# Kernel tuning notes

Hardware: AMD Instinct MI355X
Metric: run time of the kernel (lower is better)

The kernel has to match this reference:

```python
import jax, jax.numpy as jnp
import numpy as np

HIDDEN = 768
HEADS = 12
HEAD_DIM = HIDDEN // HEADS
SCALE = HEAD_DIM ** -0.5
B, S = 8, 1024


def _qkv(x, Wqkv):
    # x: [b, s, H] -> q, k, v each [b, heads, s, d]
    h = jnp.einsum('bsh,hk->bsk', x, Wqkv)          # [b, s, 3*H]
    h = h.reshape(x.shape[0], x.shape[1], 3, HEADS, HEAD_DIM)
    h = jnp.transpose(h, (2, 0, 3, 1, 4))           # [3, b, heads, s, d]
    return h[0], h[1], h[2]


def _attn(q, k, v):
    # q,k,v: [b, heads, s, d]
    att = jax.nn.softmax(jnp.einsum('bhxd,bhyd->bhxy', q, k) * SCALE, axis=-1)
    return jnp.einsum('bhxy,bhyd->bhxd', att, v)


def _out(o, Wout, bout):
    # o: [b, heads, s, d] -> [b, s, H]
    b, h, s, d = o.shape
    o = jnp.transpose(o, (0, 2, 1, 3)).reshape(b, s, h * d)
    return jnp.einsum('bsh,hk->bsk', o, Wout) + bout


def setup_inputs() -> dict:
    key = jax.random.key(0)
    k1, k2, k3, k4, k5 = jax.random.split(key, 5)
    x = jax.random.normal(k1, (B, S, HIDDEN), dtype=jnp.float32)
    x2 = jax.random.normal(k2, (B, S, HIDDEN), dtype=jnp.float32)
    Wqkv = jax.random.normal(k3, (HIDDEN, 3 * HIDDEN), dtype=jnp.float32) * (HIDDEN ** -0.5)
    Wout = jax.random.normal(k4, (HIDDEN, HIDDEN), dtype=jnp.float32) * (HIDDEN ** -0.5)
    bout = jax.random.normal(k5, (HIDDEN,), dtype=jnp.float32) * 0.01
    return {'x': x, 'x2': x2, 'Wqkv': Wqkv, 'Wout': Wout, 'bout': bout}


def reference(x, x2, Wqkv, Wout, bout):
    q, k, v = _qkv(x, Wqkv)
    q2, k2, v2 = _qkv(x2, Wqkv)
    o1 = _attn(q, k, v)      # self-attention on x
    o2 = _attn(q2, k2, v2)   # self-attention on x2
    o3 = _attn(q, k2, v2)    # cross-attention: queries from x, keys/values from x2
    y1 = _out(o1, Wout, bout)
    y2 = _out(o2, Wout, bout)
    y3 = _out(o3, Wout, bout)
    return (y1, y2, y3)
```

## Files before the change

### kernel.cpp

```cpp
#include <hip/hip_runtime.h>
#include <math.h>


#define HIDDEN 768
#define NH 12
#define HD 64
#define BB 8
#define SS 1024
#define ATT_SCALE 0.125f

typedef unsigned short u16;
typedef unsigned int u32;
typedef __attribute__((ext_vector_type(8))) short short8;
typedef __attribute__((ext_vector_type(4))) float f32x4;

constexpr int MROWS = BB * SS;
constexpr int M_QKV = 2 * MROWS;
constexpr int N_QKV = 3 * HIDDEN;
constexpr long QKV_ELEMS = (long)BB * NH * SS * HD;
constexpr long AX_ELEMS  = (long)M_QKV * HIDDEN;
constexpr long O_ELEMS   = (long)3 * MROWS * HIDDEN;
constexpr long WQT_ELEMS = (long)N_QKV * HIDDEN;
constexpr size_t OFF2 = (size_t)12 * QKV_ELEMS * 2;

__device__ inline u16 f2bf(float x) {
    u32 u = __float_as_uint(x);
    return (u16)((u + 0x7FFFu + ((u >> 16) & 1u)) >> 16);
}
__device__ inline float bf2f(u16 h) { return __uint_as_float(((u32)h) << 16); }
__device__ inline int swz(int row, int bcol) {
    return ((row << 7) + bcol) ^ ((row & 7) << 4);
}
__device__ inline int swzV(int row, int bcol) {
    return ((row << 7) + bcol) ^ ((((row >> 3) ^ row) & 7) << 4);
}
#define MFMA16(a, b, c) __builtin_amdgcn_mfma_f32_16x16x32_bf16(a, b, c, 0, 0, 0)

__device__ inline void gload16(const u16* g, u16* l) {
    __builtin_amdgcn_global_load_lds(
        (const __attribute__((address_space(1))) u32*)g,
        (__attribute__((address_space(3))) u32*)l, 16, 0, 0);
}

__global__ __launch_bounds__(256) void conv_x_kernel(
    const float* __restrict__ x, const float* __restrict__ x2,
    u16* __restrict__ axh, u16* __restrict__ axl)
{
    const size_t HALF = (size_t)MROWS * HIDDEN;
    const size_t NTOT = (size_t)AX_ELEMS;
    const size_t step = (size_t)gridDim.x * 256 * 4;
    for (size_t e = ((size_t)blockIdx.x * 256 + threadIdx.x) * 4; e < NTOT; e += step) {
        const float4 v = (e < HALF) ? *(const float4*)&x[e]
                                    : *(const float4*)&x2[e - HALF];
        ushort4 h, l;
        h.x = f2bf(v.x); l.x = f2bf(v.x - bf2f(h.x));
        h.y = f2bf(v.y); l.y = f2bf(v.y - bf2f(h.y));
        h.z = f2bf(v.z); l.z = f2bf(v.z - bf2f(h.z));
        h.w = f2bf(v.w); l.w = f2bf(v.w - bf2f(h.w));
        *(ushort4*)&axh[e] = h;
        *(ushort4*)&axl[e] = l;
    }
}

__global__ __launch_bounds__(256) void conv_wt_kernel(
    const float* __restrict__ Wqkv, const float* __restrict__ Wout,
    u16* __restrict__ wqt_h, u16* __restrict__ wqt_l,
    u16* __restrict__ wot_h, u16* __restrict__ wot_l)
{
    __shared__ float T[64][65];
    const int bk = blockIdx.x;
    int bn = blockIdx.y;
    const float* W; int ncols; u16 *oh, *ol;
    if (bn < 36) { W = Wqkv; ncols = N_QKV; oh = wqt_h; ol = wqt_l; }
    else         { W = Wout; ncols = HIDDEN; oh = wot_h; ol = wot_l; bn -= 36; }
    const int k0 = bk * 64, n0 = bn * 64;
    const int t = threadIdx.x;
    {
        const int r = t >> 2, c0 = (t & 3) * 16;
        #pragma unroll
        for (int q = 0; q < 4; ++q) {
            const float4 v = *(const float4*)&W[(size_t)(k0 + r) * ncols + n0 + c0 + q * 4];
            T[r][c0 + q * 4 + 0] = v.x;
            T[r][c0 + q * 4 + 1] = v.y;
            T[r][c0 + q * 4 + 2] = v.z;
            T[r][c0 + q * 4 + 3] = v.w;
        }
    }
    __syncthreads();
    {
        const int n = t >> 2, kk0 = (t & 3) * 16;
        const size_t ob = (size_t)(n0 + n) * HIDDEN + k0 + kk0;
        #pragma unroll
        for (int q = 0; q < 4; ++q) {
            ushort4 h, l;
            float v0 = T[kk0 + q * 4 + 0][n];
            float v1 = T[kk0 + q * 4 + 1][n];
            float v2 = T[kk0 + q * 4 + 2][n];
            float v3 = T[kk0 + q * 4 + 3][n];
            h.x = f2bf(v0); l.x = f2bf(v0 - bf2f(h.x));
            h.y = f2bf(v1); l.y = f2bf(v1 - bf2f(h.y));
            h.z = f2bf(v2); l.z = f2bf(v2 - bf2f(h.z));
            h.w = f2bf(v3); l.w = f2bf(v3 - bf2f(h.w));
            *(ushort4*)&oh[ob + q * 4] = h;
            *(ushort4*)&ol[ob + q * 4] = l;
        }
    }
}

__global__ __launch_bounds__(256)
__attribute__((amdgpu_waves_per_eu(2, 2)))
void gemm_qkv_mfma(const u16* __restrict__ Agh, const u16* __restrict__ Agl,
                   const u16* __restrict__ Bgh, const u16* __restrict__ Bgl,
                   u16* __restrict__ planes)
{
    __shared__ u16 LAh[4096], LAl[4096], LBh[4096], LBl[4096];

    const int tid = threadIdx.x, lane = tid & 63, wid = tid >> 6;
    const int l15 = lane & 15, lg = lane >> 4;
    const int wr = wid >> 1, wc = wid & 1;
    const int m0 = blockIdx.x * 128, n0 = blockIdx.y * 128;

    const f32x4 fz = {0.f, 0.f, 0.f, 0.f};
    f32x4 acc[4][4] = {{fz,fz,fz,fz},{fz,fz,fz,fz},{fz,fz,fz,fz},{fz,fz,fz,fz}};

    for (int kt = 0; kt < HIDDEN / 32; ++kt) {
        const int k0 = kt * 32;
        __syncthreads();
        #pragma unroll
        for (int u = 0; u < 2; ++u) {
            const int s   = (wid * 2 + u) * 64 + lane;
            const int row = s >> 2;
            const int kc  = (s & 3) * 8;
            const int lo  = (wid * 2 + u) * 512;
            const size_t ga = (size_t)(m0 + row) * HIDDEN + k0 + kc;
            const size_t gb = (size_t)(n0 + row) * HIDDEN + k0 + kc;
            gload16(Agh + ga, &LAh[lo]);
            gload16(Agl + ga, &LAl[lo]);
            gload16(Bgh + gb, &LBh[lo]);
            gload16(Bgl + gb, &LBl[lo]);
        }
        __syncthreads();

        short8 ah[4], al[4], bh[4], bl[4];
        #pragma unroll
        for (int i = 0; i < 4; ++i) {
            const int ro = (wr * 64 + i * 16 + l15) * 32 + lg * 8;
            ah[i] = *(const short8*)&LAh[ro];
            al[i] = *(const short8*)&LAl[ro];
        }
        #pragma unroll
        for (int j = 0; j < 4; ++j) {
            const int ro = (wc * 64 + j * 16 + l15) * 32 + lg * 8;
            bh[j] = *(const short8*)&LBh[ro];
            bl[j] = *(const short8*)&LBl[ro];
        }
        #pragma unroll
        for (int i = 0; i < 4; ++i)
            #pragma unroll
            for (int j = 0; j < 4; ++j) {
                acc[i][j] = MFMA16(ah[i], bh[j], acc[i][j]);
                acc[i][j] = MFMA16(ah[i], bl[j], acc[i][j]);
                acc[i][j] = MFMA16(al[i], bh[j], acc[i][j]);
            }
    }

    #pragma unroll
    for (int i = 0; i < 4; ++i) {
        #pragma unroll
        for (int r = 0; r < 4; ++r) {
            const int mr  = m0 + wr * 64 + i * 16 + lg * 4 + r;
            const int inp = (mr >= MROWS) ? 1 : 0;
            const int mm  = mr & (MROWS - 1);
            const int bb  = mm >> 10, ssr = mm & (SS - 1);
            #pragma unroll
            for (int j = 0; j < 4; ++j) {
                const int n   = n0 + wc * 64 + j * 16 + l15;
                const int sel = n / HIDDEN;
                const int hh  = (n % HIDDEN) >> 6;
                const int dd  = n & 63;
                const float v = acc[i][j][r];
                const u16 vh = f2bf(v);
                const u16 vl = f2bf(v - bf2f(vh));
                u16* ph = planes + (size_t)(inp * 6 + sel * 2) * QKV_ELEMS;
                const size_t idx = (((size_t)bb * NH + hh) * SS + ssr) * HD + dd;
                ph[idx] = vh;
                ph[QKV_ELEMS + idx] = vl;
            }
        }
    }
}

__global__ __launch_bounds__(256)
__attribute__((amdgpu_waves_per_eu(2, 2)))
void attn_mfma_kernel(const u16* __restrict__ planes,
                      u16* __restrict__ o_h, u16* __restrict__ o_l)
{
    __shared__ u16 Khi[64 * 64], Klo[64 * 64];
    __shared__ u16 Vthi[64 * 64], Vtlo[64 * 64];
    __shared__ u16 Pbuf[4][2][2][16 * 64];

    const int tid  = threadIdx.x;
    const int lane = tid & 63, wid = tid >> 6;
    const int l15  = lane & 15, lg = lane >> 4;

    const int work = (blockIdx.x & 7) * 288 + (blockIdx.x >> 3);
    const int qt   = work & 7;
    const int bh   = (work >> 3) % 96;
    const int aid  = (work >> 3) / 96;

    const int qinp  = (aid == 1) ? 1 : 0;
    const int kvinp = (aid == 0) ? 0 : 1;
    const size_t base = (size_t)bh * SS * HD;

    const u16* __restrict__ qhi = planes + (size_t)(qinp * 6 + 0) * QKV_ELEMS;
    const u16* __restrict__ qlo = qhi + QKV_ELEMS;
    const u16* __restrict__ khi = planes + (size_t)(kvinp * 6 + 2) * QKV_ELEMS;
    const u16* __restrict__ klo = khi + QKV_ELEMS;
    const u16* __restrict__ vhi = planes + (size_t)(kvinp * 6 + 4) * QKV_ELEMS;
    const u16* __restrict__ vlo = vhi + QKV_ELEMS;

    const int qb = qt * 128 + wid * 32;
    short8 qfh[2][2], qfl[2][2];
    #pragma unroll
    for (int g = 0; g < 2; ++g)
        #pragma unroll
        for (int dk = 0; dk < 2; ++dk) {
            const size_t off = base + (size_t)(qb + g * 16 + l15) * HD + dk * 32 + lg * 8;
            qfh[g][dk] = *(const short8*)&qhi[off];
            qfl[g][dk] = *(const short8*)&qlo[off];
        }

    const f32x4 fz = {0.f, 0.f, 0.f, 0.f};
    f32x4 O[2][4] = {{fz, fz, fz, fz}, {fz, fz, fz, fz}};
    float mrun[2] = {-INFINITY, -INFINITY};
    float lrun[2] = {0.f, 0.f};

    for (int kt0 = 0; kt0 < SS; kt0 += 64) {
        __syncthreads();
        {
            #pragma unroll
            for (int i = 0; i < 2; ++i) {
                const int c  = tid + 256 * i;
                const int ky = c >> 3, dg = (c & 7) * 8;
                const size_t g = base + (size_t)(kt0 + ky) * HD + dg;
                const int b = swz(ky, dg * 2);
                *(short8*)((char*)Khi + b) = *(const short8*)&khi[g];
                *(short8*)((char*)Klo + b) = *(const short8*)&klo[g];
            }
            const int kp = tid >> 3;
            const int d0 = (tid & 7) * 8;
            const size_t g0 = base + (size_t)(kt0 + 2 * kp) * HD + d0;
            short8 vah = *(const short8*)&vhi[g0];
            short8 vbh = *(const short8*)&vhi[g0 + HD];
            short8 val = *(const short8*)&vlo[g0];
            short8 vbl = *(const short8*)&vlo[g0 + HD];
            #pragma unroll
            for (int i = 0; i < 8; ++i) {
                const int d = d0 + i;
                const int b = swzV(d, kp * 4);
                *(u32*)((char*)Vthi + b) = (u32)(u16)vah[i] | ((u32)(u16)vbh[i] << 16);
                *(u32*)((char*)Vtlo + b) = (u32)(u16)val[i] | ((u32)(u16)vbl[i] << 16);
            }
        }
        __syncthreads();

        f32x4 S[2][4] = {{fz, fz, fz, fz}, {fz, fz, fz, fz}};
        #pragma unroll
        for (int dk = 0; dk < 2; ++dk) {
            #pragma unroll
            for (int kt = 0; kt < 4; ++kt) {
                const int b = swz(kt * 16 + l15, dk * 64 + lg * 16);
                short8 kfh = *(const short8*)((char*)Khi + b);
                short8 kfl = *(const short8*)((char*)Klo + b);
                #pragma unroll
                for (int g = 0; g < 2; ++g) {
                    S[g][kt] = MFMA16(kfh, qfh[g][dk], S[g][kt]);
                    S[g][kt] = MFMA16(kfl, qfh[g][dk], S[g][kt]);
                    S[g][kt] = MFMA16(kfh, qfl[g][dk], S[g][kt]);
                }
            }
        }

        #pragma unroll
        for (int g = 0; g < 2; ++g) {
            float pm = -INFINITY;
            #pragma unroll
            for (int kt = 0; kt < 4; ++kt)
                #pragma unroll
                for (int r = 0; r < 4; ++r) {
                    S[g][kt][r] *= ATT_SCALE;
                    pm = fmaxf(pm, S[g][kt][r]);
                }
            pm = fmaxf(pm, __shfl_xor(pm, 16, 64));
            pm = fmaxf(pm, __shfl_xor(pm, 32, 64));
            const float mnew = fmaxf(mrun[g], pm);
            const float corr = __expf(mrun[g] - mnew);
            mrun[g] = mnew;
            lrun[g] *= corr;

            u16* __restrict__ Ph = &Pbuf[wid][g][0][0];
            u16* __restrict__ Pl = &Pbuf[wid][g][1][0];
            float psum = 0.f;
            #pragma unroll
            for (int kt = 0; kt < 4; ++kt) {
                float p0 = __expf(S[g][kt][0] - mnew);
                float p1 = __expf(S[g][kt][1] - mnew);
                float p2 = __expf(S[g][kt][2] - mnew);
                float p3 = __expf(S[g][kt][3] - mnew);
                psum += (p0 + p1) + (p2 + p3);
                const u32 u0 = __float_as_uint(p0), u1 = __float_as_uint(p1);
                const u32 u2 = __float_as_uint(p2), u3 = __float_as_uint(p3);
                const u32 hpk0 = (u0 >> 16) | (u1 & 0xFFFF0000u);
                const u32 hpk1 = (u2 >> 16) | (u3 & 0xFFFF0000u);
                const float l0 = p0 - __uint_as_float(u0 & 0xFFFF0000u);
                const float l1 = p1 - __uint_as_float(u1 & 0xFFFF0000u);
                const float l2 = p2 - __uint_as_float(u2 & 0xFFFF0000u);
                const float l3 = p3 - __uint_as_float(u3 & 0xFFFF0000u);
                const u32 lpk0 = (__float_as_uint(l0) >> 16) | (__float_as_uint(l1) & 0xFFFF0000u);
                const u32 lpk1 = (__float_as_uint(l2) >> 16) | (__float_as_uint(l3) & 0xFFFF0000u);
                const int b0 = swz(l15, kt * 32 + lg * 8);
                *(u32*)((char*)Ph + b0)     = hpk0;
                *(u32*)((char*)Ph + b0 + 4) = hpk1;
                *(u32*)((char*)Pl + b0)     = lpk0;
                *(u32*)((char*)Pl + b0 + 4) = lpk1;
            }
            psum += __shfl_xor(psum, 16, 64);
            psum += __shfl_xor(psum, 32, 64);
            lrun[g] += psum;

            #pragma unroll
            for (int r = 0; r < 4; ++r) {
                const float c = __shfl(corr, lg * 4 + r, 64);
                #pragma unroll
                for (int dn = 0; dn < 4; ++dn) O[g][dn][r] *= c;
            }
        }

        #pragma unroll
        for (int ch = 0; ch < 2; ++ch) {
            short8 vfh[4], vfl[4];
            #pragma unroll
            for (int dn = 0; dn < 4; ++dn) {
                const int vb = swzV(dn * 16 + l15, ch * 64 + lg * 16);
                vfh[dn] = *(const short8*)((char*)Vthi + vb);
                vfl[dn] = *(const short8*)((char*)Vtlo + vb);
            }
            #pragma unroll
            for (int g = 0; g < 2; ++g) {
                const int pb = swz(l15, ch * 64 + lg * 16);
                short8 pah = *(const short8*)((char*)&Pbuf[wid][g][0][0] + pb);
                short8 pal = *(const short8*)((char*)&Pbuf[wid][g][1][0] + pb);
                #pragma unroll
                for (int dn = 0; dn < 4; ++dn) {
                    O[g][dn] = MFMA16(pah, vfh[dn], O[g][dn]);
                    O[g][dn] = MFMA16(pah, vfl[dn], O[g][dn]);
                    O[g][dn] = MFMA16(pal, vfh[dn], O[g][dn]);
                }
            }
        }
    }

    const int b = bh / NH, h = bh % NH;
    #pragma unroll
    for (int g = 0; g < 2; ++g) {
        const float linv = 1.f / lrun[g];
        #pragma unroll
        for (int r = 0; r < 4; ++r) {
            const float inv = __shfl(linv, lg * 4 + r, 64);
            const int grow = aid * MROWS + b * SS + qb + g * 16 + lg * 4 + r;
            const size_t rb = (size_t)grow * HIDDEN + h * HD;
            #pragma unroll
            for (int dn = 0; dn < 4; ++dn) {
                const float v = O[g][dn][r] * inv;
                const u16 vh = f2bf(v);
                o_h[rb + dn * 16 + l15] = vh;
                o_l[rb + dn * 16 + l15] = f2bf(v - bf2f(vh));
            }
        }
    }
}

__global__ __launch_bounds__(256)
__attribute__((amdgpu_waves_per_eu(2, 2)))
void gemm_out_mfma(const u16* __restrict__ Agh, const u16* __restrict__ Agl,
                   const u16* __restrict__ Bgh, const u16* __restrict__ Bgl,
                   const float* __restrict__ bias, float* __restrict__ out)
{
    __shared__ u16 LAh[4096], LAl[4096], LBh[4096], LBl[4096];

    const int tid = threadIdx.x, lane = tid & 63, wid = tid >> 6;
    const int l15 = lane & 15, lg = lane >> 4;
    const int wr = wid >> 1, wc = wid & 1;
    const int m0 = blockIdx.x * 128, n0 = blockIdx.y * 128;

    const f32x4 fz = {0.f, 0.f, 0.f, 0.f};
    f32x4 acc[4][4] = {{fz,fz,fz,fz},{fz,fz,fz,fz},{fz,fz,fz,fz},{fz,fz,fz,fz}};

    for (int kt = 0; kt < HIDDEN / 32; ++kt) {
        const int k0 = kt * 32;
        __syncthreads();
        #pragma unroll
        for (int u = 0; u < 2; ++u) {
            const int s   = (wid * 2 + u) * 64 + lane;
            const int row = s >> 2;
            const int kc  = (s & 3) * 8;
            const int lo  = (wid * 2 + u) * 512;
            const size_t ga = (size_t)(m0 + row) * HIDDEN + k0 + kc;
            const size_t gb = (size_t)(n0 + row) * HIDDEN + k0 + kc;
            gload16(Agh + ga, &LAh[lo]);
            gload16(Agl + ga, &LAl[lo]);
            gload16(Bgh + gb, &LBh[lo]);
            gload16(Bgl + gb, &LBl[lo]);
        }
        __syncthreads();

        short8 ah[4], al[4], bh[4], bl[4];
        #pragma unroll
        for (int i = 0; i < 4; ++i) {
            const int ro = (wr * 64 + i * 16 + l15) * 32 + lg * 8;
            ah[i] = *(const short8*)&LAh[ro];
            al[i] = *(const short8*)&LAl[ro];
        }
        #pragma unroll
        for (int j = 0; j < 4; ++j) {
            const int ro = (wc * 64 + j * 16 + l15) * 32 + lg * 8;
            bh[j] = *(const short8*)&LBh[ro];
            bl[j] = *(const short8*)&LBl[ro];
        }
        #pragma unroll
        for (int i = 0; i < 4; ++i)
            #pragma unroll
            for (int j = 0; j < 4; ++j) {
                acc[i][j] = MFMA16(ah[i], bh[j], acc[i][j]);
                acc[i][j] = MFMA16(ah[i], bl[j], acc[i][j]);
                acc[i][j] = MFMA16(al[i], bh[j], acc[i][j]);
            }
    }

    #pragma unroll
    for (int i = 0; i < 4; ++i) {
        #pragma unroll
        for (int r = 0; r < 4; ++r) {
            const int mr = m0 + wr * 64 + i * 16 + lg * 4 + r;
            #pragma unroll
            for (int j = 0; j < 4; ++j) {
                const int n = n0 + wc * 64 + j * 16 + l15;
                out[(size_t)mr * HIDDEN + n] = acc[i][j][r] + bias[n];
            }
        }
    }
}

extern "C" void kernel_launch(void* const* d_in, const int* in_sizes, int n_in,
                              void* d_out, int out_size, void* d_ws, size_t ws_size,
                              hipStream_t stream)
{
    const float* x    = (const float*)d_in[0];
    const float* x2   = (const float*)d_in[1];
    const float* Wqkv = (const float*)d_in[2];
    const float* Wout = (const float*)d_in[3];
    const float* bout = (const float*)d_in[4];
    float* out = (float*)d_out;

    char* wsb = (char*)d_ws;
    u16* planes = (u16*)wsb;
    u16* ax_h  = (u16*)(wsb + OFF2);
    u16* ax_l  = ax_h + AX_ELEMS;
    u16* wqt_h = ax_l + AX_ELEMS;
    u16* wqt_l = wqt_h + WQT_ELEMS;
    u16* o_h   = (u16*)(wsb + OFF2);
    u16* o_l   = o_h + O_ELEMS;
    u16* wot_h = o_l + O_ELEMS;
    u16* wot_l = wot_h + (long)HIDDEN * HIDDEN;

    conv_x_kernel<<<3072, 256, 0, stream>>>(x, x2, ax_h, ax_l);

    dim3 gw(12, 48);
    conv_wt_kernel<<<gw, 256, 0, stream>>>(Wqkv, Wout, wqt_h, wqt_l, wot_h, wot_l);

    dim3 g1(M_QKV / 128, N_QKV / 128);
    gemm_qkv_mfma<<<g1, 256, 0, stream>>>(ax_h, ax_l, wqt_h, wqt_l, planes);

    attn_mfma_kernel<<<2304, 256, 0, stream>>>(planes, o_h, o_l);

    dim3 g3(3 * MROWS / 128, HIDDEN / 128);
    gemm_out_mfma<<<g3, 256, 0, stream>>>(o_h, o_l, wot_h, wot_l, bout, out);
}
```

Measured before the change: 662.4 us.

## Double-buffer GEMM LDS tiles and add lazy softmax rescaling in attention

Both projection GEMMs now use two LDS buffers, issuing the next K-tile's global-to-LDS loads before the current tile's MFMAs, with one barrier per iteration. The attention kernel now rescales the running max and output accumulator only when some row's new max exceeds the stored one by more than 8, which skips the per-tile exp and shuffle rescale work. P-tile stores are also merged into 64-bit writes. Costs: the GEMM LDS footprint doubles, which may limit occupancy. The lazy rescale lets exponentials reach up to e^8 before renormalising, which shifts the split-bf16 precision of P slightly.

Measured after the change: 702.4 us. 1.06x slower.

```diff
diff --git a/kernel.cpp b/kernel.cpp
--- a/kernel.cpp
+++ b/kernel.cpp
@@ -113,19 +113,15 @@
                    const u16* __restrict__ Bgh, const u16* __restrict__ Bgl,
                    u16* __restrict__ planes)
 {
-    __shared__ u16 LAh[4096], LAl[4096], LBh[4096], LBl[4096];
+    __shared__ u16 LAh[2][4096], LAl[2][4096], LBh[2][4096], LBl[2][4096];
 
     const int tid = threadIdx.x, lane = tid & 63, wid = tid >> 6;
     const int l15 = lane & 15, lg = lane >> 4;
     const int wr = wid >> 1, wc = wid & 1;
     const int m0 = blockIdx.x * 128, n0 = blockIdx.y * 128;
 
-    const f32x4 fz = {0.f, 0.f, 0.f, 0.f};
-    f32x4 acc[4][4] = {{fz,fz,fz,fz},{fz,fz,fz,fz},{fz,fz,fz,fz},{fz,fz,fz,fz}};
-
-    for (int kt = 0; kt < HIDDEN / 32; ++kt) {
+    auto stage = [&](int kt, int bf) {
         const int k0 = kt * 32;
-        __syncthreads();
         #pragma unroll
         for (int u = 0; u < 2; ++u) {
             const int s   = (wid * 2 + u) * 64 + lane;
@@ -134,25 +130,35 @@
             const int lo  = (wid * 2 + u) * 512;
             const size_t ga = (size_t)(m0 + row) * HIDDEN + k0 + kc;
             const size_t gb = (size_t)(n0 + row) * HIDDEN + k0 + kc;
-            gload16(Agh + ga, &LAh[lo]);
-            gload16(Agl + ga, &LAl[lo]);
-            gload16(Bgh + gb, &LBh[lo]);
-            gload16(Bgl + gb, &LBl[lo]);
-        }
-        __syncthreads();
+            gload16(Agh + ga, &LAh[bf][lo]);
+            gload16(Agl + ga, &LAl[bf][lo]);
+            gload16(Bgh + gb, &LBh[bf][lo]);
+            gload16(Bgl + gb, &LBl[bf][lo]);
+        }
+    };
+
+    const f32x4 fz = {0.f, 0.f, 0.f, 0.f};
+    f32x4 acc[4][4] = {{fz,fz,fz,fz},{fz,fz,fz,fz},{fz,fz,fz,fz},{fz,fz,fz,fz}};
+
+    stage(0, 0);
+    __syncthreads();
+
+    int bf = 0;
+    for (int kt = 0; kt < HIDDEN / 32; ++kt) {
+        if (kt + 1 < HIDDEN / 32) stage(kt + 1, bf ^ 1);
 
         short8 ah[4], al[4], bh[4], bl[4];
         #pragma unroll
         for (int i = 0; i < 4; ++i) {
             const int ro = (wr * 64 + i * 16 + l15) * 32 + lg * 8;
-            ah[i] = *(const short8*)&LAh[ro];
-            al[i] = *(const short8*)&LAl[ro];
+            ah[i] = *(const short8*)&LAh[bf][ro];
+            al[i] = *(const short8*)&LAl[bf][ro];
         }
         #pragma unroll
         for (int j = 0; j < 4; ++j) {
             const int ro = (wc * 64 + j * 16 + l15) * 32 + lg * 8;
-            bh[j] = *(const short8*)&LBh[ro];
-            bl[j] = *(const short8*)&LBl[ro];
+            bh[j] = *(const short8*)&LBh[bf][ro];
+            bl[j] = *(const short8*)&LBl[bf][ro];
         }
         #pragma unroll
         for (int i = 0; i < 4; ++i)
@@ -162,6 +168,8 @@
                 acc[i][j] = MFMA16(ah[i], bl[j], acc[i][j]);
                 acc[i][j] = MFMA16(al[i], bh[j], acc[i][j]);
             }
+        __syncthreads();
+        bf ^= 1;
     }
 
     #pragma unroll
@@ -293,20 +301,30 @@
                 }
             pm = fmaxf(pm, __shfl_xor(pm, 16, 64));
             pm = fmaxf(pm, __shfl_xor(pm, 32, 64));
-            const float mnew = fmaxf(mrun[g], pm);
-            const float corr = __expf(mrun[g] - mnew);
-            mrun[g] = mnew;
-            lrun[g] *= corr;
+
+            if (__any(pm - mrun[g] > 8.f)) {
+                const float mnew = fmaxf(mrun[g], pm);
+                const float corr = __expf(mrun[g] - mnew);
+                lrun[g] *= corr;
+                #pragma unroll
+                for (int r = 0; r < 4; ++r) {
+                    const float c = __shfl(corr, lg * 4 + r, 64);
+                    #pragma unroll
+                    for (int dn = 0; dn < 4; ++dn) O[g][dn][r] *= c;
+                }
+                mrun[g] = mnew;
+            }
+            const float mref = mrun[g];
 
             u16* __restrict__ Ph = &Pbuf[wid][g][0][0];
             u16* __restrict__ Pl = &Pbuf[wid][g][1][0];
             float psum = 0.f;
             #pragma unroll
             for (int kt = 0; kt < 4; ++kt) {
-                float p0 = __expf(S[g][kt][0] - mnew);
-                float p1 = __expf(S[g][kt][1] - mnew);
-                float p2 = __expf(S[g][kt][2] - mnew);
-                float p3 = __expf(S[g][kt][3] - mnew);
+                float p0 = __expf(S[g][kt][0] - mref);
+                float p1 = __expf(S[g][kt][1] - mref);
+                float p2 = __expf(S[g][kt][2] - mref);
+                float p3 = __expf(S[g][kt][3] - mref);
                 psum += (p0 + p1) + (p2 + p3);
                 const u32 u0 = __float_as_uint(p0), u1 = __float_as_uint(p1);
                 const u32 u2 = __float_as_uint(p2), u3 = __float_as_uint(p3);
@@ -319,21 +337,12 @@
                 const u32 lpk0 = (__float_as_uint(l0) >> 16) | (__float_as_uint(l1) & 0xFFFF0000u);
                 const u32 lpk1 = (__float_as_uint(l2) >> 16) | (__float_as_uint(l3) & 0xFFFF0000u);
                 const int b0 = swz(l15, kt * 32 + lg * 8);
-                *(u32*)((char*)Ph + b0)     = hpk0;
-                *(u32*)((char*)Ph + b0 + 4) = hpk1;
-                *(u32*)((char*)Pl + b0)     = lpk0;
-                *(u32*)((char*)Pl + b0 + 4) = lpk1;
+                *(uint2*)((char*)Ph + b0) = make_uint2(hpk0, hpk1);
+                *(uint2*)((char*)Pl + b0) = make_uint2(lpk0, lpk1);
             }
             psum += __shfl_xor(psum, 16, 64);
             psum += __shfl_xor(psum, 32, 64);
             lrun[g] += psum;
-
-            #pragma unroll
-            for (int r = 0; r < 4; ++r) {
-                const float c = __shfl(corr, lg * 4 + r, 64);
-                #pragma unroll
-                for (int dn = 0; dn < 4; ++dn) O[g][dn][r] *= c;
-            }
         }
 
         #pragma unroll
@@ -386,19 +395,15 @@
                    const u16* __restrict__ Bgh, const u16* __restrict__ Bgl,
                    const float* __restrict__ bias, float* __restrict__ out)
 {
-    __shared__ u16 LAh[4096], LAl[4096], LBh[4096], LBl[4096];
+    __shared__ u16 LAh[2][4096], LAl[2][4096], LBh[2][4096], LBl[2][4096];
 
     const int tid = threadIdx.x, lane = tid & 63, wid = tid >> 6;
     const int l15 = lane & 15, lg = lane >> 4;
     const int wr = wid >> 1, wc = wid & 1;
     const int m0 = blockIdx.x * 128, n0 = blockIdx.y * 128;
 
-    const f32x4 fz = {0.f, 0.f, 0.f, 0.f};
-    f32x4 acc[4][4] = {{fz,fz,fz,fz},{fz,fz,fz,fz},{fz,fz,fz,fz},{fz,fz,fz,fz}};
-
-    for (int kt = 0; kt < HIDDEN / 32; ++kt) {
+    auto stage = [&](int kt, int bf) {
         const int k0 = kt * 32;
-        __syncthreads();
         #pragma unroll
         for (int u = 0; u < 2; ++u) {
             const int s   = (wid * 2 + u) * 64 + lane;
@@ -407,25 +412,35 @@
             const int lo  = (wid * 2 + u) * 512;
             const size_t ga = (size_t)(m0 + row) * HIDDEN + k0 + kc;
             const size_t gb = (size_t)(n0 + row) * HIDDEN + k0 + kc;
-            gload16(Agh + ga, &LAh[lo]);
-            gload16(Agl + ga, &LAl[lo]);
-            gload16(Bgh + gb, &LBh[lo]);
-            gload16(Bgl + gb, &LBl[lo]);
-        }
-        __syncthreads();
+            gload16(Agh + ga, &LAh[bf][lo]);
+            gload16(Agl + ga, &LAl[bf][lo]);
+            gload16(Bgh + gb, &LBh[bf][lo]);
+            gload16(Bgl + gb, &LBl[bf][lo]);
+        }
+    };
+
+    const f32x4 fz = {0.f, 0.f, 0.f, 0.f};
+    f32x4 acc[4][4] = {{fz,fz,fz,fz},{fz,fz,fz,fz},{fz,fz,fz,fz},{fz,fz,fz,fz}};
+
+    stage(0, 0);
+    __syncthreads();
+
+    int bf = 0;
+    for (int kt = 0; kt < HIDDEN / 32; ++kt) {
+        if (kt + 1 < HIDDEN / 32) stage(kt + 1, bf ^ 1);
 
         short8 ah[4], al[4], bh[4], bl[4];
         #pragma unroll
         for (int i = 0; i < 4; ++i) {
             const int ro = (wr * 64 + i * 16 + l15) * 32 + lg * 8;
-            ah[i] = *(const short8*)&LAh[ro];
-            al[i] = *(const short8*)&LAl[ro];
+            ah[i] = *(const short8*)&LAh[bf][ro];
+            al[i] = *(const short8*)&LAl[bf][ro];
         }
         #pragma unroll
         for (int j = 0; j < 4; ++j) {
             const int ro = (wc * 64 + j * 16 + l15) * 32 + lg * 8;
-            bh[j] = *(const short8*)&LBh[ro];
-            bl[j] = *(const short8*)&LBl[ro];
+            bh[j] = *(const short8*)&LBh[bf][ro];
+            bl[j] = *(const short8*)&LBl[bf][ro];
         }
         #pragma unroll
         for (int i = 0; i < 4; ++i)
@@ -435,6 +450,8 @@
                 acc[i][j] = MFMA16(ah[i], bl[j], acc[i][j]);
                 acc[i][j] = MFMA16(al[i], bh[j], acc[i][j]);
             }
+        __syncthreads();
+        bf ^= 1;
     }
 
     #pragma unroll
```
